# Kernel optimization log

Measured on AMD Instinct MI355X. Metric: run time of the kernel, lower is better.

## Reference

```python
import jax, jax.numpy as jnp
import numpy as np

B, S, E = 4, 2048, 1024
H = 4
DH = E // H          # 256 head dim
DQ = E // 4          # 256 quaternion d_model
ALPHA = 1.5
EPS = 1e-10
FOCUS = 0.9
SEL = 2.0


def setup_inputs() -> dict:
    key = jax.random.key(0)
    ks = jax.random.split(key, 6)
    sc = 0.02
    return {
        "x": jax.random.normal(ks[0], (B, S, E), dtype=jnp.float32),
        "in_proj_w": jax.random.normal(ks[1], (3 * E, E), dtype=jnp.float32) * sc,
        "in_proj_b": jnp.zeros((3 * E,), dtype=jnp.float32),
        "out_w": jax.random.normal(ks[2], (E, E), dtype=jnp.float32) * sc,
        "out_b": jnp.zeros((E,), dtype=jnp.float32),
        "m_w1": jax.random.normal(ks[3], (E, E), dtype=jnp.float32) * sc,
        "m_b1": jnp.zeros((E,), dtype=jnp.float32),
        "m_w2": jax.random.normal(ks[4], (E, E), dtype=jnp.float32) * sc,
        "m_b2": jnp.zeros((E,), dtype=jnp.float32),
    }


def quaternion_multiply(q1, q2):
    # Hamilton product over last dim of size 4 (complex-valued components).
    w1, x1, y1, z1 = q1[..., 0], q1[..., 1], q1[..., 2], q1[..., 3]
    w2, x2, y2, z2 = q2[..., 0], q2[..., 1], q2[..., 2], q2[..., 3]
    return jnp.stack([
        w1 * w2 - x1 * x2 - y1 * y2 - z1 * z2,
        w1 * x2 + x1 * w2 + y1 * z2 - z1 * y2,
        w1 * y2 - x1 * z2 + y1 * w2 + z1 * x2,
        w1 * z2 + x1 * y2 - y1 * x2 + z1 * w2,
    ], axis=-1)


def _mha(x, in_proj_w, in_proj_b, out_w, out_b):
    # torch nn.MultiheadAttention self-attention, batch_first
    qkv = x @ in_proj_w.T + in_proj_b              # [B,S,3E]
    q, k, v = jnp.split(qkv, 3, axis=-1)
    q = q.reshape(B, S, H, DH)
    k = k.reshape(B, S, H, DH)
    v = v.reshape(B, S, H, DH)
    scores = jnp.einsum('bqhd,bkhd->bhqk', q, k) / jnp.sqrt(jnp.float32(DH))
    attn = jax.nn.softmax(scores, axis=-1)
    out = jnp.einsum('bhqk,bkhd->bqhd', attn, v).reshape(B, S, E)
    return out @ out_w.T + out_b


def _spectral_attention(signal):
    sq = signal.reshape(B, S, DQ, 4)
    sfft = jnp.fft.fft(sq, axis=-3)                 # complex64, FFT over seq
    kk = jnp.arange(S, dtype=jnp.float32)
    filt = jnp.exp(1j * ALPHA * jnp.arctan(jnp.log(kk + EPS)))  # [S] complex
    sf = sfft * filt[None, :, None, None]
    inter = quaternion_multiply(quaternion_multiply(sf, sf), sf)
    attended = jnp.fft.ifft(inter, axis=-3).real
    return attended.reshape(B, S, E)


def reference(x, in_proj_w, in_proj_b, out_w, out_b, m_w1, m_b1, m_w2, m_b2):
    nicotinic = _mha(x, in_proj_w, in_proj_b, out_w, out_b)
    h = jax.nn.gelu(x @ m_w1.T + m_b1, approximate=False)
    muscarinic = h @ m_w2.T + m_b2
    chol = FOCUS * nicotinic + (1.0 - FOCUS) * muscarinic
    attn_w = _spectral_attention(chol * SEL)
    return x * attn_w
```

## Files before the change

kernel.cpp:

```cpp
#include <hip/hip_runtime.h>
#include <cstdint>

typedef _Float16 f16;
typedef unsigned short u16;
typedef __attribute__((ext_vector_type(8))) _Float16 half8;
typedef __attribute__((ext_vector_type(2))) __fp16 fp16x2;
typedef __attribute__((ext_vector_type(4))) float f32x4;

#define MFMA_F16(a, b, c) __builtin_amdgcn_mfma_f32_16x16x32_f16(a, b, c, 0, 0, 0)

#define WAITVM8() asm volatile("s_waitcnt vmcnt(8)" ::: "memory")
#define WAITVM4() asm volatile("s_waitcnt vmcnt(4)" ::: "memory")
#define WAITVM0() asm volatile("s_waitcnt vmcnt(0)" ::: "memory")
#define BARRIER() do { asm volatile("" ::: "memory"); __builtin_amdgcn_s_barrier(); \
                       asm volatile("" ::: "memory"); } while (0)

__device__ inline void stage16(const void* g, void* l) {
#if defined(__has_builtin) && __has_builtin(__builtin_amdgcn_global_load_lds)
  __builtin_amdgcn_global_load_lds(
      (const __attribute__((address_space(1))) unsigned*)g,
      (__attribute__((address_space(3))) unsigned*)l, 16, 0, 0);
#else
  *(int4*)l = *(const int4*)g;
#endif
}

__device__ inline int pack_f16(float a, float b) {
#if defined(__has_builtin) && __has_builtin(__builtin_amdgcn_cvt_pkrtz)
  union { fp16x2 h; int i; } u;
  u.h = __builtin_amdgcn_cvt_pkrtz(a, b);
  return u.i;
#else
  union { f16 h[2]; int i; } u;
  u.h[0] = (f16)a; u.h[1] = (f16)b;
  return u.i;
#endif
}

__global__ __launch_bounds__(256)
void conv_all(const float* __restrict__ x, const float* __restrict__ wqkv,
              const float* __restrict__ wout, const float* __restrict__ w1,
              const float* __restrict__ w2, f16* __restrict__ dst) {
  int i = (blockIdx.x * 256 + threadIdx.x) * 8;
  const float* src; int off;
  if (i < 8388608)       { src = x;    off = i; }
  else if (i < 11534336) { src = wqkv; off = i - 8388608; }
  else if (i < 12582912) { src = wout; off = i - 11534336; }
  else if (i < 13631488) { src = w1;   off = i - 12582912; }
  else                   { src = w2;   off = i - 13631488; }
  float4 a = *(const float4*)(src + off);
  float4 b = *(const float4*)(src + off + 4);
  half8 h;
  h[0] = (f16)a.x; h[1] = (f16)a.y; h[2] = (f16)a.z; h[3] = (f16)a.w;
  h[4] = (f16)b.x; h[5] = (f16)b.y; h[6] = (f16)b.z; h[7] = (f16)b.w;
  *(half8*)(dst + i) = h;
}

template<int EPI, int OUTF16>
__global__ __launch_bounds__(256, 2)
void gemm_f16(const f16* __restrict__ A, const f16* __restrict__ W,
              const float* __restrict__ bias, void* __restrict__ Cv,
              int N, int K, const float* __restrict__ aux) {
  __shared__ __align__(16) f16 lds[2][16384];
  const int tid = threadIdx.x;
  const int lane = tid & 63, w = tid >> 6;
  const int g = lane >> 4, lm = lane & 15;
  const int wr = w >> 1, wc = w & 1;
  const int m0 = blockIdx.y * 128, n0 = blockIdx.x * 128;

  const f16* src[8];
#pragma unroll
  for (int j = 0; j < 8; ++j) {
    int u = j * 256 + tid;
    if (u < 1024) {
      int row = u >> 3, s = u & 7;
      src[j] = A + (size_t)(m0 + row) * K + ((s ^ (row & 7)) << 3);
    } else {
      int v = u - 1024;
      int row = v >> 3, s = v & 7;
      src[j] = W + (size_t)(n0 + row) * K + ((s ^ (row & 7)) << 3);
    }
  }

  f32x4 acc[4][4];
#pragma unroll
  for (int mt = 0; mt < 4; ++mt)
#pragma unroll
    for (int nt = 0; nt < 4; ++nt) acc[mt][nt] = (f32x4){0.f, 0.f, 0.f, 0.f};

#pragma unroll
  for (int j = 0; j < 8; ++j) stage16(src[j], &lds[0][(j * 256 + tid) * 8]);
  __syncthreads();

  const int KT = K >> 6;
#pragma unroll 1
  for (int t = 0; t < KT; ++t) {
    const f16* bufA = lds[t & 1];
    const f16* bufB = bufA + 8192;
    if (t + 1 < KT) {
#pragma unroll
      for (int j = 0; j < 8; ++j) {
        src[j] += 64;
        stage16(src[j], &lds[(t + 1) & 1][(j * 256 + tid) * 8]);
      }
      WAITVM8();
    } else {
      WAITVM0();
    }
    BARRIER();
#pragma unroll
    for (int ks = 0; ks < 2; ++ks) {
      half8 a[4], b[4];
#pragma unroll
      for (int mt = 0; mt < 4; ++mt) {
        int row = wr * 64 + mt * 16 + lm;
        a[mt] = *(const half8*)(bufA + row * 64 + (((ks * 4 + g) ^ (row & 7)) << 3));
      }
#pragma unroll
      for (int nt = 0; nt < 4; ++nt) {
        int row = wc * 64 + nt * 16 + lm;
        b[nt] = *(const half8*)(bufB + row * 64 + (((ks * 4 + g) ^ (row & 7)) << 3));
      }
#pragma unroll
      for (int mt = 0; mt < 4; ++mt)
#pragma unroll
        for (int nt = 0; nt < 4; ++nt)
          acc[mt][nt] = MFMA_F16(a[mt], b[nt], acc[mt][nt]);
    }
    BARRIER();
  }

  const int crow = m0 + wr * 64 + g * 4;
  const int ccol = n0 + wc * 64 + lm;
#pragma unroll
  for (int nt = 0; nt < 4; ++nt) {
    float bb = bias[ccol + nt * 16];
#pragma unroll
    for (int mt = 0; mt < 4; ++mt) {
#pragma unroll
      for (int r = 0; r < 4; ++r) {
        size_t idx = (size_t)(crow + mt * 16 + r) * N + ccol + nt * 16;
        float v = acc[mt][nt][r] + bb;
        if (EPI == 1) v = 0.5f * v * (1.0f + erff(v * 0.70710678118654752f));
        if (EPI == 2) v = (0.9f * aux[idx] + 0.1f * v) * 2.0f;
        if (OUTF16) ((f16*)Cv)[idx] = (f16)v;
        else        ((float*)Cv)[idx] = v;
      }
    }
  }
}

__global__ __launch_bounds__(256)
void vtrans(const f16* __restrict__ qkv, f16* __restrict__ Vt) {
  __shared__ unsigned vlds[64][65];
  const int tid = threadIdx.x;
  const int bh = blockIdx.x >> 5, st = blockIdx.x & 31;
  const int b = bh >> 2, h = bh & 3;
  const int s0 = st * 64;
  const u16* q16 = (const u16*)qkv;
  u16* v16 = (u16*)Vt;
#pragma unroll 1
  for (int dc = 0; dc < 4; ++dc) {
    __syncthreads();
#pragma unroll 1
    for (int i = 0; i < 16; ++i) {
      int idx = i * 256 + tid;
      int s = idx >> 6, dl = idx & 63;
      vlds[dl][s] = q16[(size_t)(b * 2048 + s0 + s) * 3072 + 2048 + h * 256 + dc * 64 + dl];
    }
    __syncthreads();
#pragma unroll 1
    for (int i = 0; i < 16; ++i) {
      int idx = i * 256 + tid;
      int dl = idx >> 6, s = idx & 63;
      v16[((size_t)bh * 256 + dc * 64 + dl) * 2048 + s0 + s] = (u16)vlds[dl][s];
    }
  }
}

__global__ __launch_bounds__(256, 2)
void flash_f16(const f16* __restrict__ qkv, const f16* __restrict__ Vt,
               f16* __restrict__ attn) {
  __shared__ __align__(16) f16 lds[32768];
  const int tid = threadIdx.x;
  const int lane = tid & 63, w = tid >> 6;
  const int g = lane >> 4, lm = lane & 15;
  const int raw = blockIdx.x;
  const int bh = (raw & 7) * 2 + (raw >> 8);
  const int qt = (raw >> 3) & 31;
  const int b = bh >> 2, h = bh & 3;
  const int q0 = qt * 64 + w * 16;
  const float SC = 0.09016844005555896f;

  half8 qf[8];
  {
    const f16* qp = qkv + (size_t)(b * 2048 + q0 + lm) * 3072 + h * 256 + g * 8;
#pragma unroll
    for (int c = 0; c < 8; ++c) qf[c] = *(const half8*)(qp + c * 32);
  }

  const f16* kbase = qkv + (size_t)b * 2048 * 3072 + 1024 + h * 256;
  const f16* vbase = Vt + (size_t)bh * 256 * 2048;
  int kofs[4], vofs[4];
#pragma unroll
  for (int j = 0; j < 4; ++j) {
    int u = j * 256 + tid;
    int kv = u >> 5, s = u & 31;
    kofs[j] = kv * 3072 + ((s ^ (kv & 7)) << 3);
    int d = u >> 2, sl = u & 3;
    vofs[j] = d * 2048 + ((sl ^ ((d >> 1) & 3)) << 3);
  }

  f32x4 o[16];
#pragma unroll
  for (int f = 0; f < 16; ++f) o[f] = (f32x4){0.f, 0.f, 0.f, 0.f};
  float m = -3e38f, l = 0.f;
  half8 paP = (half8){0, 0, 0, 0, 0, 0, 0, 0};

#pragma unroll
  for (int j = 0; j < 4; ++j) stage16(kbase + kofs[j], &lds[(j * 256 + tid) * 8]);

#pragma unroll 1
  for (int t = 0; t < 64; ++t) {
    const int cb_ = t & 1;
    if (t < 63) {
      const int kt = (t + 1) * 98304;
#pragma unroll
      for (int j = 0; j < 4; ++j)
        stage16(kbase + kofs[j] + kt, &lds[(cb_ ^ 1) * 8192 + (j * 256 + tid) * 8]);
    }
    {
      const int vt_ = t * 32;
#pragma unroll
      for (int j = 0; j < 4; ++j)
        stage16(vbase + vofs[j] + vt_, &lds[16384 + cb_ * 8192 + (j * 256 + tid) * 8]);
    }
    if (t < 63) { WAITVM8(); } else { WAITVM4(); }
    BARRIER();

    const f16* kb = &lds[cb_ * 8192];

    f32x4 s0 = {0.f, 0.f, 0.f, 0.f}, s1 = {0.f, 0.f, 0.f, 0.f};
    __builtin_amdgcn_s_setprio(1);
#pragma unroll
    for (int c = 0; c < 8; ++c) {
      int slot = ((c * 4 + g) ^ (lm & 7)) << 3;
      half8 b0 = *(const half8*)(kb + lm * 256 + slot);
      half8 b1 = *(const half8*)(kb + (16 + lm) * 256 + slot);
      s0 = MFMA_F16(b0, qf[c], s0);
      s1 = MFMA_F16(b1, qf[c], s1);
    }
    __builtin_amdgcn_s_setprio(0);

    if (t > 0) {
      const f16* vbp = &lds[16384 + (cb_ ^ 1) * 8192];
      __builtin_amdgcn_s_setprio(1);
#pragma unroll
      for (int f = 0; f < 16; ++f) {
        int d = f * 16 + lm;
        half8 bv = *(const half8*)(vbp + d * 32 + ((g ^ ((d >> 1) & 3)) << 3));
        o[f] = MFMA_F16(paP, bv, o[f]);
      }
      __builtin_amdgcn_s_setprio(0);
    }

    float a0[4], a1[4];
#pragma unroll
    for (int r = 0; r < 4; ++r) { a0[r] = s0[r] * SC; a1[r] = s1[r] * SC; }
    float mx = fmaxf(fmaxf(fmaxf(a0[0], a0[1]), fmaxf(a0[2], a0[3])),
                     fmaxf(fmaxf(a1[0], a1[1]), fmaxf(a1[2], a1[3])));
    mx = fmaxf(mx, __shfl_xor(mx, 16));
    mx = fmaxf(mx, __shfl_xor(mx, 32));

    if (!__all(mx <= m + 8.0f)) {
      float mn = fmaxf(m, mx);
      float corr = exp2f(m - mn);
      m = mn; l *= corr;
#pragma unroll
      for (int r = 0; r < 4; ++r) {
        float cr = __shfl(corr, ((lane >> 2) & 12) + r);
#pragma unroll
        for (int f = 0; f < 16; ++f) o[f][r] *= cr;
      }
    }

    float e0[4], e1[4], rs;
#pragma unroll
    for (int r = 0; r < 4; ++r) { e0[r] = exp2f(a0[r] - m); e1[r] = exp2f(a1[r] - m); }
    rs = ((e0[0] + e0[1]) + (e0[2] + e0[3])) + ((e1[0] + e1[1]) + (e1[2] + e1[3]));
    rs += __shfl_xor(rs, 16);
    rs += __shfl_xor(rs, 32);
    l += rs;

    int A01 = pack_f16(e0[0], e0[1]);
    int A23 = pack_f16(e0[2], e0[3]);
    int B01 = pack_f16(e1[0], e1[1]);
    int B23 = pack_f16(e1[2], e1[3]);
    const int s1l = ((lane & 16) << 1) + lm;
    const int s2l = s1l + 16;
    int t0a = __shfl(A01, s1l), t0b = __shfl(B01, s1l);
    int t1a = __shfl(A23, s1l), t1b = __shfl(B23, s1l);
    int t2a = __shfl(A01, s2l), t2b = __shfl(B01, s2l);
    int t3a = __shfl(A23, s2l), t3b = __shfl(B23, s2l);
    union { int i[4]; half8 h; } pau;
    const bool hi = lane >= 32;
    pau.i[0] = hi ? t0b : t0a;
    pau.i[1] = hi ? t1b : t1a;
    pau.i[2] = hi ? t2b : t2a;
    pau.i[3] = hi ? t3b : t3a;
    paP = pau.h;

    BARRIER();
  }

  WAITVM0();
  BARRIER();
  {
    const f16* vbp = &lds[16384 + 8192];
#pragma unroll
    for (int f = 0; f < 16; ++f) {
      int d = f * 16 + lm;
      half8 bv = *(const half8*)(vbp + d * 32 + ((g ^ ((d >> 1) & 3)) << 3));
      o[f] = MFMA_F16(paP, bv, o[f]);
    }
  }

  float inv[4];
#pragma unroll
  for (int r = 0; r < 4; ++r) inv[r] = 1.0f / __shfl(l, ((lane >> 2) & 12) + r);
#pragma unroll
  for (int f = 0; f < 16; ++f)
#pragma unroll
    for (int r = 0; r < 4; ++r)
      attn[(size_t)(b * 2048 + q0 + g * 4 + r) * 1024 + h * 256 + f * 16 + lm] =
          (f16)(o[f][r] * inv[r]);
}

__device__ inline float2 cmul(float2 a, float2 b) {
  return make_float2(a.x * b.x - a.y * b.y, a.x * b.y + a.y * b.x);
}
__device__ inline float2 cmulc(float2 a, float2 b) {
  return make_float2(a.x * b.x + a.y * b.y, a.y * b.x - a.x * b.y);
}
__device__ inline void qcube(float2& w, float2& x, float2& y, float2& z, float2 f) {
  w = cmul(w, f); x = cmul(x, f); y = cmul(y, f); z = cmul(z, f);
  float2 a2 = cmul(w, w);
  float2 sx = cmul(x, x), sy = cmul(y, y), sz = cmul(z, z);
  float2 s = make_float2(sx.x + sy.x + sz.x, sx.y + sy.y + sz.y);
  float2 t3 = make_float2(a2.x - 3.f * s.x, a2.y - 3.f * s.y);
  float2 cf = make_float2(3.f * a2.x - s.x, 3.f * a2.y - s.y);
  w = cmul(w, t3); x = cmul(cf, x); y = cmul(cf, y); z = cmul(cf, z);
}

__device__ inline int fftpos(int k) {
  int kp = k >> 1;
  return ((k & 1) << 10) | ((kp & 3) << 8) | ((kp & 12) << 4) | (kp & 48)
       | ((kp >> 4) & 12) | ((kp >> 8) & 3);
}

__global__ __launch_bounds__(256)
void spectral4(const float* __restrict__ chol, const float* __restrict__ xin,
               float* __restrict__ outp) {
  __shared__ __align__(16) float2 Z[2][2048];
  __shared__ float2 tw[1024];
  const int tid = threadIdx.x;
  const int b = blockIdx.x >> 8;
  const int qd = blockIdx.x & 255;
  const size_t c0 = (size_t)qd * 4;
  const float* cb = chol + (size_t)b * 2048 * 1024;

  for (int j = tid; j < 1024; j += 256) {
    float ang = -6.2831853071795864769f * (float)j * (1.0f / 2048.0f);
    float sv, cv; sincosf(ang, &sv, &cv);
    tw[j] = make_float2(cv, sv);
  }
  for (int s = tid; s < 2048; s += 256) {
    float4 v = *(const float4*)(cb + (size_t)s * 1024 + c0);
    Z[0][s] = make_float2(v.x, v.y);
    Z[1][s] = make_float2(v.z, v.w);
  }
  __syncthreads();

#pragma unroll 1
  for (int it = 0; it < 8; ++it) {
    int gg = it * 256 + tid;
    int c = gg >> 10, j = gg & 1023;
    float2 a = Z[c][j], bb = Z[c][j + 1024];
    Z[c][j] = make_float2(a.x + bb.x, a.y + bb.y);
    Z[c][j + 1024] = cmul(make_float2(a.x - bb.x, a.y - bb.y), tw[j]);
  }
  __syncthreads();

#pragma unroll 1
  for (int lq = 8; lq >= 0; lq -= 2) {
    const int Q = 1 << lq, st = 512 >> lq;
#pragma unroll 1
    for (int it = 0; it < 4; ++it) {
      int gg = it * 256 + tid;
      int c = gg >> 9, bf = gg & 511;
      int j = bf & (Q - 1);
      int base = ((bf >> lq) << (lq + 2)) | j;
      float2 a = Z[c][base], bq = Z[c][base + Q];
      float2 cc = Z[c][base + 2 * Q], d = Z[c][base + 3 * Q];
      float2 t0 = make_float2(a.x + cc.x, a.y + cc.y);
      float2 t1 = make_float2(a.x - cc.x, a.y - cc.y);
      float2 t2 = make_float2(bq.x + d.x, bq.y + d.y);
      float2 bd = make_float2(bq.x - d.x, bq.y - d.y);
      float2 t3 = make_float2(bd.y, -bd.x);
      float2 y0 = make_float2(t0.x + t2.x, t0.y + t2.y);
      float2 y1 = make_float2(t1.x + t3.x, t1.y + t3.y);
      float2 y2 = make_float2(t0.x - t2.x, t0.y - t2.y);
      float2 y3 = make_float2(t1.x - t3.x, t1.y - t3.y);
      int i3 = 3 * j * st;
      float sg = (i3 & 1024) ? -1.f : 1.f;
      i3 &= 1023;
      Z[c][base] = y0;
      Z[c][base + Q] = cmul(y1, tw[j * st]);
      Z[c][base + 2 * Q] = cmul(y2, tw[2 * j * st]);
      float2 r3 = cmul(y3, tw[i3]);
      Z[c][base + 3 * Q] = make_float2(r3.x * sg, r3.y * sg);
    }
    __syncthreads();
  }

#pragma unroll 1
  for (int it = 0; it < 4; ++it) {
    int jj = it * 256 + tid;
    int nrep = (jj == 0) ? 2 : 1;
#pragma unroll 1
    for (int rep = 0; rep < nrep; ++rep) {
      int k  = (jj == 0) ? (rep ? 1024 : 0) : jj;
      int kn = (jj == 0) ? k : 2048 - jj;
      int p  = fftpos(k);
      int pp = fftpos(kn);
      float2 z0p = Z[0][p], z0q = Z[0][pp];
      float2 z1p = Z[1][p], z1q = Z[1][pp];
      float2 wk = make_float2(0.5f * (z0p.x + z0q.x), 0.5f * (z0p.y - z0q.y));
      float2 xk = make_float2(0.5f * (z0p.y + z0q.y), 0.5f * (z0q.x - z0p.x));
      float2 yk = make_float2(0.5f * (z1p.x + z1q.x), 0.5f * (z1p.y - z1q.y));
      float2 zk = make_float2(0.5f * (z1p.y + z1q.y), 0.5f * (z1q.x - z1p.x));
      float2 wn = make_float2(0.5f * (z0q.x + z0p.x), 0.5f * (z0q.y - z0p.y));
      float2 xn = make_float2(0.5f * (z0q.y + z0p.y), 0.5f * (z0p.x - z0q.x));
      float2 yn = make_float2(0.5f * (z1q.x + z1p.x), 0.5f * (z1q.y - z1p.y));
      float2 zn = make_float2(0.5f * (z1q.y + z1p.y), 0.5f * (z1p.x - z1q.x));
      float sk, ck, sn, cn;
      sincosf(1.5f * atanf(logf((float)k + 1e-10f)), &sk, &ck);
      sincosf(1.5f * atanf(logf((float)kn + 1e-10f)), &sn, &cn);
      qcube(wk, xk, yk, zk, make_float2(ck, sk));
      qcube(wn, xn, yn, zn, make_float2(cn, sn));
      Z[0][p]  = make_float2(0.5f * (wk.x + wn.x) - 0.5f * (xk.y - xn.y),
                             0.5f * (wk.y - wn.y) + 0.5f * (xk.x + xn.x));
      Z[0][pp] = make_float2(0.5f * (wn.x + wk.x) - 0.5f * (xn.y - xk.y),
                             0.5f * (wn.y - wk.y) + 0.5f * (xn.x + xk.x));
      Z[1][p]  = make_float2(0.5f * (yk.x + yn.x) - 0.5f * (zk.y - zn.y),
                             0.5f * (yk.y - yn.y) + 0.5f * (zk.x + zn.x));
      Z[1][pp] = make_float2(0.5f * (yn.x + yk.x) - 0.5f * (zn.y - zk.y),
                             0.5f * (yn.y - yk.y) + 0.5f * (zn.x + zk.x));
    }
  }
  __syncthreads();

#pragma unroll 1
  for (int lq = 0; lq <= 8; lq += 2) {
    const int Q = 1 << lq, st = 512 >> lq;
#pragma unroll 1
    for (int it = 0; it < 4; ++it) {
      int gg = it * 256 + tid;
      int c = gg >> 9, bf = gg & 511;
      int j = bf & (Q - 1);
      int base = ((bf >> lq) << (lq + 2)) | j;
      float2 a = Z[c][base];
      float2 bq = cmulc(Z[c][base + Q], tw[j * st]);
      float2 cc = cmulc(Z[c][base + 2 * Q], tw[2 * j * st]);
      int i3 = 3 * j * st;
      float sg = (i3 & 1024) ? -1.f : 1.f;
      i3 &= 1023;
      float2 d = cmulc(Z[c][base + 3 * Q], tw[i3]);
      d = make_float2(d.x * sg, d.y * sg);
      float2 t0 = make_float2(a.x + cc.x, a.y + cc.y);
      float2 t1 = make_float2(a.x - cc.x, a.y - cc.y);
      float2 t2 = make_float2(bq.x + d.x, bq.y + d.y);
      float2 bd = make_float2(bq.x - d.x, bq.y - d.y);
      float2 t3 = make_float2(-bd.y, bd.x);
      Z[c][base]         = make_float2(t0.x + t2.x, t0.y + t2.y);
      Z[c][base + Q]     = make_float2(t1.x + t3.x, t1.y + t3.y);
      Z[c][base + 2 * Q] = make_float2(t0.x - t2.x, t0.y - t2.y);
      Z[c][base + 3 * Q] = make_float2(t1.x - t3.x, t1.y - t3.y);
    }
    __syncthreads();
  }

#pragma unroll 1
  for (int it = 0; it < 8; ++it) {
    int gg = it * 256 + tid;
    int c = gg >> 10, j = gg & 1023;
    float2 a = Z[c][j];
    float2 bw = cmulc(Z[c][j + 1024], tw[j]);
    Z[c][j] = make_float2(a.x + bw.x, a.y + bw.y);
    Z[c][j + 1024] = make_float2(a.x - bw.x, a.y - bw.y);
  }
  __syncthreads();

  const float* xb = xin + (size_t)b * 2048 * 1024;
  float* ob = outp + (size_t)b * 2048 * 1024;
  const float inv = 1.0f / 2048.0f;
  for (int s = tid; s < 2048; s += 256) {
    float4 xv = *(const float4*)(xb + (size_t)s * 1024 + c0);
    float2 r0 = Z[0][s], r1 = Z[1][s];
    float4 o;
    o.x = xv.x * r0.x * inv;
    o.y = xv.y * r0.y * inv;
    o.z = xv.z * r1.x * inv;
    o.w = xv.w * r1.y * inv;
    *(float4*)(ob + (size_t)s * 1024 + c0) = o;
  }
}

extern "C" void kernel_launch(void* const* d_in, const int* in_sizes, int n_in,
                              void* d_out, int out_size, void* d_ws, size_t ws_size,
                              hipStream_t stream) {
  const float* x    = (const float*)d_in[0];
  const float* wqkv = (const float*)d_in[1];
  const float* bqkv = (const float*)d_in[2];
  const float* wout = (const float*)d_in[3];
  const float* bout = (const float*)d_in[4];
  const float* w1   = (const float*)d_in[5];
  const float* b1   = (const float*)d_in[6];
  const float* w2   = (const float*)d_in[7];
  const float* b2   = (const float*)d_in[8];
  float* out = (float*)d_out;
  char* wsb = (char*)d_ws;
  const size_t MB = 1048576;

  f16*   xf    = (f16*)(wsb);
  f16*   wqf   = (f16*)(wsb + 16 * MB);
  f16*   wof   = (f16*)(wsb + 22 * MB);
  f16*   w1f   = (f16*)(wsb + 24 * MB);
  f16*   w2f   = (f16*)(wsb + 26 * MB);
  f16*   qkvF  = (f16*)(wsb + 28 * MB);
  f16*   VtF   = (f16*)(wsb + 76 * MB);
  f16*   attnF = (f16*)(wsb + 92 * MB);
  float* nico  = (float*)(wsb + 108 * MB);
  f16*   hF    = (f16*)(wsb + 140 * MB);
  float* chol  = (float*)(wsb + 156 * MB);

  conv_all<<<7168, 256, 0, stream>>>(x, wqkv, wout, w1, w2, xf);

  gemm_f16<0, 1><<<dim3(24, 64), 256, 0, stream>>>(xf, wqf, bqkv, qkvF, 3072, 1024, nullptr);
  vtrans<<<512, 256, 0, stream>>>(qkvF, VtF);
  flash_f16<<<512, 256, 0, stream>>>(qkvF, VtF, attnF);
  gemm_f16<0, 0><<<dim3(8, 64), 256, 0, stream>>>(attnF, wof, bout, nico, 1024, 1024, nullptr);
  gemm_f16<1, 1><<<dim3(8, 64), 256, 0, stream>>>(xf, w1f, b1, hF, 1024, 1024, nullptr);
  gemm_f16<2, 0><<<dim3(8, 64), 256, 0, stream>>>(hF, w2f, b2, chol, 1024, 1024, nico);
  spectral4<<<1024, 256, 0, stream>>>(chol, x, out);
}
```

Baseline: 416.7 us.

## Merge QKV with MLP-up GEMM and fold out-proj and MLP-down into one K=2048 GEMM

```diff
diff --git a/kernel.cpp b/kernel.cpp
--- a/kernel.cpp
+++ b/kernel.cpp
@@ -39,28 +39,33 @@
 
 __global__ __launch_bounds__(256)
 void conv_all(const float* __restrict__ x, const float* __restrict__ wqkv,
-              const float* __restrict__ wout, const float* __restrict__ w1,
+              const float* __restrict__ w1, const float* __restrict__ wout,
               const float* __restrict__ w2, f16* __restrict__ dst) {
   int i = (blockIdx.x * 256 + threadIdx.x) * 8;
-  const float* src; int off;
-  if (i < 8388608)       { src = x;    off = i; }
-  else if (i < 11534336) { src = wqkv; off = i - 8388608; }
-  else if (i < 12582912) { src = wout; off = i - 11534336; }
-  else if (i < 13631488) { src = w1;   off = i - 12582912; }
-  else                   { src = w2;   off = i - 13631488; }
-  float4 a = *(const float4*)(src + off);
-  float4 b = *(const float4*)(src + off + 4);
+  const float* src; size_t dofs; float sc = 1.0f;
+  if (i < 8388608)       { src = x + i;               dofs = i; }
+  else if (i < 11534336) { src = wqkv + (i - 8388608); dofs = i; }
+  else if (i < 12582912) { src = w1 + (i - 11534336);  dofs = i; }
+  else if (i < 13631488) {
+    int t = i - 12582912; int j = t >> 10, k = t & 1023;
+    src = wout + t; dofs = 12582912 + (size_t)j * 2048 + k; sc = 1.8f;
+  } else {
+    int t = i - 13631488; int j = t >> 10, k = t & 1023;
+    src = w2 + t; dofs = 12582912 + (size_t)j * 2048 + 1024 + k; sc = 0.2f;
+  }
+  float4 a = *(const float4*)src;
+  float4 b = *(const float4*)(src + 4);
   half8 h;
-  h[0] = (f16)a.x; h[1] = (f16)a.y; h[2] = (f16)a.z; h[3] = (f16)a.w;
-  h[4] = (f16)b.x; h[5] = (f16)b.y; h[6] = (f16)b.z; h[7] = (f16)b.w;
-  *(half8*)(dst + i) = h;
-}
-
-template<int EPI, int OUTF16>
+  h[0] = (f16)(a.x * sc); h[1] = (f16)(a.y * sc); h[2] = (f16)(a.z * sc); h[3] = (f16)(a.w * sc);
+  h[4] = (f16)(b.x * sc); h[5] = (f16)(b.y * sc); h[6] = (f16)(b.z * sc); h[7] = (f16)(b.w * sc);
+  *(half8*)(dst + dofs) = h;
+}
+
+template<int EPI>
 __global__ __launch_bounds__(256, 2)
 void gemm_f16(const f16* __restrict__ A, const f16* __restrict__ W,
-              const float* __restrict__ bias, void* __restrict__ Cv,
-              int N, int K, const float* __restrict__ aux) {
+              const float* __restrict__ bias0, const float* __restrict__ bias1,
+              void* __restrict__ out0, void* __restrict__ out1, int N, int K) {
   __shared__ __align__(16) f16 lds[2][16384];
   const int tid = threadIdx.x;
   const int lane = tid & 63, w = tid >> 6;
@@ -132,20 +137,46 @@
 
   const int crow = m0 + wr * 64 + g * 4;
   const int ccol = n0 + wc * 64 + lm;
-#pragma unroll
-  for (int nt = 0; nt < 4; ++nt) {
-    float bb = bias[ccol + nt * 16];
-#pragma unroll
-    for (int mt = 0; mt < 4; ++mt) {
-#pragma unroll
-      for (int r = 0; r < 4; ++r) {
-        size_t idx = (size_t)(crow + mt * 16 + r) * N + ccol + nt * 16;
-        float v = acc[mt][nt][r] + bb;
-        if (EPI == 1) v = 0.5f * v * (1.0f + erff(v * 0.70710678118654752f));
-        if (EPI == 2) v = (0.9f * aux[idx] + 0.1f * v) * 2.0f;
-        if (OUTF16) ((f16*)Cv)[idx] = (f16)v;
-        else        ((float*)Cv)[idx] = v;
-      }
+  if (EPI == 3) {
+    if (n0 < 3072) {
+      f16* qk = (f16*)out0;
+#pragma unroll
+      for (int nt = 0; nt < 4; ++nt) {
+        float bb = bias0[ccol + nt * 16];
+#pragma unroll
+        for (int mt = 0; mt < 4; ++mt)
+#pragma unroll
+          for (int r = 0; r < 4; ++r)
+            qk[(size_t)(crow + mt * 16 + r) * 3072 + ccol + nt * 16] =
+                (f16)(acc[mt][nt][r] + bb);
+      }
+    } else {
+      f16* cat = (f16*)out1;
+      const int hc = ccol - 3072;
+#pragma unroll
+      for (int nt = 0; nt < 4; ++nt) {
+        float bb = bias1[hc + nt * 16];
+#pragma unroll
+        for (int mt = 0; mt < 4; ++mt)
+#pragma unroll
+          for (int r = 0; r < 4; ++r) {
+            float v = acc[mt][nt][r] + bb;
+            v = 0.5f * v * (1.0f + erff(v * 0.70710678118654752f));
+            cat[(size_t)(crow + mt * 16 + r) * 2048 + 1024 + hc + nt * 16] = (f16)v;
+          }
+      }
+    }
+  } else {
+    float* ch = (float*)out0;
+#pragma unroll
+    for (int nt = 0; nt < 4; ++nt) {
+      float bb = 1.8f * bias0[ccol + nt * 16] + 0.2f * bias1[ccol + nt * 16];
+#pragma unroll
+      for (int mt = 0; mt < 4; ++mt)
+#pragma unroll
+        for (int r = 0; r < 4; ++r)
+          ch[(size_t)(crow + mt * 16 + r) * 1024 + ccol + nt * 16] =
+              acc[mt][nt][r] + bb;
     }
   }
 }
@@ -332,7 +363,7 @@
   for (int f = 0; f < 16; ++f)
 #pragma unroll
     for (int r = 0; r < 4; ++r)
-      attn[(size_t)(b * 2048 + q0 + g * 4 + r) * 1024 + h * 256 + f * 16 + lm] =
+      attn[(size_t)(b * 2048 + q0 + g * 4 + r) * 2048 + h * 256 + f * 16 + lm] =
           (f16)(o[f][r] * inv[r]);
 }
 
@@ -534,23 +565,17 @@
 
   f16*   xf    = (f16*)(wsb);
   f16*   wqf   = (f16*)(wsb + 16 * MB);
-  f16*   wof   = (f16*)(wsb + 22 * MB);
-  f16*   w1f   = (f16*)(wsb + 24 * MB);
-  f16*   w2f   = (f16*)(wsb + 26 * MB);
-  f16*   qkvF  = (f16*)(wsb + 28 * MB);
-  f16*   VtF   = (f16*)(wsb + 76 * MB);
-  f16*   attnF = (f16*)(wsb + 92 * MB);
-  float* nico  = (float*)(wsb + 108 * MB);
-  f16*   hF    = (f16*)(wsb + 140 * MB);
-  float* chol  = (float*)(wsb + 156 * MB);
-
-  conv_all<<<7168, 256, 0, stream>>>(x, wqkv, wout, w1, w2, xf);
-
-  gemm_f16<0, 1><<<dim3(24, 64), 256, 0, stream>>>(xf, wqf, bqkv, qkvF, 3072, 1024, nullptr);
+  f16*   wcat  = (f16*)(wsb + 24 * MB);
+  f16*   qkvF  = (f16*)(wsb + 32 * MB);
+  f16*   VtF   = (f16*)(wsb + 80 * MB);
+  f16*   cat   = (f16*)(wsb + 96 * MB);
+  float* chol  = (float*)(wsb + 128 * MB);
+
+  conv_all<<<7168, 256, 0, stream>>>(x, wqkv, w1, wout, w2, xf);
+
+  gemm_f16<3><<<dim3(32, 64), 256, 0, stream>>>(xf, wqf, bqkv, b1, qkvF, cat, 4096, 1024);
   vtrans<<<512, 256, 0, stream>>>(qkvF, VtF);
-  flash_f16<<<512, 256, 0, stream>>>(qkvF, VtF, attnF);
-  gemm_f16<0, 0><<<dim3(8, 64), 256, 0, stream>>>(attnF, wof, bout, nico, 1024, 1024, nullptr);
-  gemm_f16<1, 1><<<dim3(8, 64), 256, 0, stream>>>(xf, w1f, b1, hF, 1024, 1024, nullptr);
-  gemm_f16<2, 0><<<dim3(8, 64), 256, 0, stream>>>(hF, w2f, b2, chol, 1024, 1024, nico);
+  flash_f16<<<512, 256, 0, stream>>>(qkvF, VtF, cat);
+  gemm_f16<4><<<dim3(8, 64), 256, 0, stream>>>(cat, wcat, bout, b2, chol, nullptr, 1024, 2048);
   spectral4<<<1024, 256, 0, stream>>>(chol, x, out);
 }
```

After: 401.5 us. 1.04x faster.
